# Performance work log

Measured on AMD Instinct MI355X. Metric: run time of the kernel, lower is better.

## Reference

```python
import jax, jax.numpy as jnp
import numpy as np

N_TOKENS = 8192
NQ = 6
NL = 2


def ry_mat(theta):
    # theta: scalar or (B,) -> (2,2) or (B,2,2) complex RY matrix
    c = jnp.cos(theta / 2)
    s = jnp.sin(theta / 2)
    return jnp.stack([jnp.stack([c, -s], -1), jnp.stack([s, c], -1)], -2).astype(jnp.complex64)


def apply_1q(state, gate, q, nq):
    # state: (B, 2**nq); gate: (2,2) shared or (B,2,2) per-batch
    B = state.shape[0]
    st = state.reshape(B, 2 ** q, 2, -1)
    if gate.ndim == 3:
        st = jnp.einsum('bij,bajc->baic', gate, st)
    else:
        st = jnp.einsum('ij,bajc->baic', gate, st)
    return st.reshape(B, -1)


def apply_rz(state, theta, q, nq):
    # diagonal RZ: multiply phases, no matmul needed
    B = state.shape[0]
    st = state.reshape(B, 2 ** q, 2, -1)
    ph = jnp.stack([jnp.exp(-0.5j * theta), jnp.exp(0.5j * theta)]).astype(jnp.complex64)
    return (st * ph[None, None, :, None]).reshape(B, -1)


def apply_cnot(state, c, t, nq):
    B = state.shape[0]
    st = state.reshape((B,) + (2,) * nq)
    s0 = jnp.take(st, 0, axis=1 + c)
    s1 = jnp.take(st, 1, axis=1 + c)
    ta = 1 + t - (1 if t > c else 0)  # target axis after removing control axis
    s1 = jnp.flip(s1, axis=ta)
    st = jnp.stack([s0, s1], axis=1 + c)
    return st.reshape(B, -1)


def prepare_states(x, params, nl, nq):
    # x: (B, nq) angles; params: (nl, nq, 2). Returns (B, 2**nq) complex statevectors.
    B = x.shape[0]
    state = jnp.zeros((B, 2 ** nq), jnp.complex64).at[:, 0].set(1.0)
    for q in range(nq):  # RY angle embedding
        state = apply_1q(state, ry_mat(x[:, q]), q, nq)
    for l in range(nl):  # PQC layers: RY, RZ rotations + CNOT ring
        for q in range(nq):
            state = apply_1q(state, ry_mat(params[l, q, 0]), q, nq)
            state = apply_rz(state, params[l, q, 1], q, nq)
        for q in range(nq):
            state = apply_cnot(state, q, (q + 1) % nq, nq)
    return state


def setup_inputs() -> dict:
    key = jax.random.key(0)
    k1, k2, k3, k4 = jax.random.split(key, 4)
    return {
        'x_tokens': jax.random.normal(k1, (N_TOKENS, NQ), dtype=jnp.float32),
        'params_q': 0.1 * jax.random.normal(k2, (NL, NQ, 2), dtype=jnp.float32),
        'params_k': 0.1 * jax.random.normal(k3, (NL, NQ, 2), dtype=jnp.float32),
        'params_v': 0.1 * jax.random.normal(k4, (NL, NQ, 2), dtype=jnp.float32),
    }


def reference(x_tokens, params_q, params_k, params_v):
    nq = x_tokens.shape[1]
    nl = params_q.shape[0]
    sq = prepare_states(x_tokens, params_q, nl, nq)  # (N, 2**nq)
    sk = prepare_states(x_tokens, params_k, nl, nq)
    ov = jnp.einsum('id,jd->ij', sq, jnp.conj(sk))  # pairwise overlaps (N, N)
    logits = jnp.real(ov * jnp.conj(ov))            # swap-test fidelity |<q|k>|^2
    attn = jax.nn.softmax(logits, axis=-1)
    sv = prepare_states(x_tokens, params_v, nl, nq)
    probs = jnp.real(sv * jnp.conj(sv))             # (N, 2**nq)
    idx = jnp.arange(2 ** nq)
    bits = (idx[None, :] >> (nq - 1 - jnp.arange(nq))[:, None]) & 1  # (nq, 2**nq)
    signs = (1.0 - 2.0 * bits).astype(probs.dtype)
    V = probs @ signs.T                              # <Z_q> per qubit -> (N, nq)
    return attn @ V
```

## Files before the change

kernel.cpp:

```cpp
#include <hip/hip_runtime.h>
#include <hip/hip_bf16.h>

#define NT 8192
#define NQB 6
#define NL 2
#define JSPLIT 16
#define JSLICE (NT / JSPLIT)
#define CHUNK 64
#define NCHUNK (JSLICE / CHUNK)
#define IPW 32
#define WPB 4
#define IPB (IPW * WPB)
#define NBI (NT / IPB)

typedef __bf16 bf16x8 __attribute__((ext_vector_type(8)));
typedef float f32x4 __attribute__((ext_vector_type(4)));

static __device__ __forceinline__ unsigned int pack_bf2(float a, float b) {
  unsigned short lo = __builtin_bit_cast(unsigned short, __float2bfloat16(a));
  unsigned short hi = __builtin_bit_cast(unsigned short, __float2bfloat16(b));
  return (unsigned int)lo | ((unsigned int)hi << 16);
}

static __device__ __forceinline__ int cnot_src(int p, int q) {
  const int mc = 1 << (5 - q);
  const int mt = 1 << (5 - ((q + 1) % NQB));
  return (p & mc) ? (p ^ mt) : p;
}

__global__ __launch_bounds__(256) void prep_kernel(
    const float* __restrict__ x, const float* __restrict__ pq,
    const float* __restrict__ pk, const float* __restrict__ pv,
    unsigned int* __restrict__ Are, unsigned int* __restrict__ Bk,
    float4* __restrict__ V4)
{
  const int wid  = blockIdx.x * 4 + (threadIdx.x >> 6);
  const int lane = threadIdx.x & 63;
  const int set  = wid >> 13;
  const int tok  = wid & (NT - 1);
  const float* pp = (set == 0) ? pq : ((set == 1) ? pk : pv);

  int m = lane;
#pragma unroll
  for (int q = 5; q >= 0; --q) m = cnot_src(m, q);
  int inv = lane;
#pragma unroll
  for (int q = 0; q < 6; ++q) inv = cnot_src(inv, q);

  float R = 1.f, phi = 0.f;
#pragma unroll
  for (int q = 0; q < 6; ++q) {
    float s, c;
    __sincosf(0.5f * (x[tok * NQB + q] + pp[q * 2 + 0]), &s, &c);
    const float bh = 0.5f * pp[q * 2 + 1];
    if ((m >> (5 - q)) & 1) { R *= s; phi += bh; }
    else                    { R *= c; phi -= bh; }
  }
  float sp, cp;
  __sincosf(phi, &sp, &cp);
  float re = R * cp, im = R * sp;

#pragma unroll
  for (int q = 0; q < 6; ++q) {
    const int mask = 1 << (5 - q);
    float s, c;
    __sincosf(0.5f * pp[2 * NQB + q * 2 + 0], &s, &c);
    const float pre = __shfl_xor(re, mask, 64);
    const float pim = __shfl_xor(im, mask, 64);
    const float se = (lane & mask) ? s : -s;
    re = fmaf(se, pre, c * re);
    im = fmaf(se, pim, c * im);
  }
  float phi2 = 0.f;
#pragma unroll
  for (int q = 0; q < 6; ++q) {
    const float bh = 0.5f * pp[2 * NQB + q * 2 + 1];
    phi2 += (lane & (1 << (5 - q))) ? bh : -bh;
  }
  float s2, c2;
  __sincosf(phi2, &s2, &c2);
  const float fre = re * c2 - im * s2;
  const float fim = re * s2 + im * c2;

  if (set == 0) {
    Are[tok * 64 + inv] = pack_bf2(fre, fim);
  } else if (set == 1) {
    Bk[tok * 64 + inv] = pack_bf2(fre, fim);
  } else {
    const float prob = fre * fre + fim * fim;
    float vq[NQB];
#pragma unroll
    for (int q = 0; q < NQB; ++q) {
      float v = (inv & (1 << (5 - q))) ? -prob : prob;
#pragma unroll
      for (int off = 1; off < 64; off <<= 1) v += __shfl_xor(v, off, 64);
      vq[q] = v;
    }
    if (lane == 0) {
      V4[tok * 2 + 0] = make_float4(vq[0], vq[1], vq[2], vq[3]);
      V4[tok * 2 + 1] = make_float4(vq[4], vq[5], 0.f, 0.f);
    }
  }
}

__global__ __launch_bounds__(256, 2) void attn_kernel(
    const uint4* __restrict__ Are, const uint4* __restrict__ Bk,
    const float4* __restrict__ V4, float* __restrict__ part)
{
  __shared__ uint4 kbuf[CHUNK * 17];
  __shared__ float4 vbuf[CHUNK * 2];

  const int tid  = threadIdx.x;
  const int lane = tid & 63;
  const int wave = tid >> 6;
  const int col  = lane & 15;
  const int quad = lane >> 4;

  const int ib = blockIdx.x & (NBI - 1);
  const int js = blockIdx.x / NBI;
  const int ibase = ib * IPB + wave * IPW;
  const int jbase0 = js * JSLICE;

  bf16x8 aRe[2][4], aIm[2][4];
#pragma unroll
  for (int rt = 0; rt < 2; ++rt) {
    const int row = ibase + rt * 16 + col;
    const uint4* pr = Are + row * 16 + quad;
#pragma unroll
    for (int s = 0; s < 4; ++s) {
      const uint4 u = pr[s * 4];
      uint4 w;
      w.x = ((u.x << 16) | (u.x >> 16)) ^ 0x80000000u;
      w.y = ((u.y << 16) | (u.y >> 16)) ^ 0x80000000u;
      w.z = ((u.z << 16) | (u.z >> 16)) ^ 0x80000000u;
      w.w = ((u.w << 16) | (u.w >> 16)) ^ 0x80000000u;
      aRe[rt][s] = __builtin_bit_cast(bf16x8, u);
      aIm[rt][s] = __builtin_bit_cast(bf16x8, w);
    }
  }

  float den[8];
  float num[8][6];
#pragma unroll
  for (int r = 0; r < 8; ++r) {
    den[r] = 0.f;
#pragma unroll
    for (int q = 0; q < 6; ++q) num[r][q] = 0.f;
  }

#pragma unroll 1
  for (int c = 0; c < NCHUNK; ++c) {
    const int jb = jbase0 + c * CHUNK;
    __syncthreads();
#pragma unroll
    for (int r = 0; r < 4; ++r) {
      const int idx = r * 256 + tid;
      kbuf[(idx >> 4) * 17 + (idx & 15)] = Bk[(jb + (idx >> 4)) * 16 + (idx & 15)];
    }
    if (tid < 2 * CHUNK) vbuf[tid] = V4[jb * 2 + tid];
    __syncthreads();

#pragma unroll
    for (int ct = 0; ct < 4; ++ct) {
      const int keyl = ct * 16 + col;
      bf16x8 bfr[4];
#pragma unroll
      for (int s = 0; s < 4; ++s)
        bfr[s] = __builtin_bit_cast(bf16x8, kbuf[keyl * 17 + s * 4 + quad]);
      const float4 v01 = vbuf[keyl * 2 + 0];
      const float4 v23 = vbuf[keyl * 2 + 1];
      const float vv[6] = {v01.x, v01.y, v01.z, v01.w, v23.x, v23.y};
#pragma unroll
      for (int rt = 0; rt < 2; ++rt) {
        f32x4 aR = {0.f, 0.f, 0.f, 0.f};
        f32x4 aI = {0.f, 0.f, 0.f, 0.f};
#pragma unroll
        for (int s = 0; s < 4; ++s) {
          aR = __builtin_amdgcn_mfma_f32_16x16x32_bf16(aRe[rt][s], bfr[s], aR, 0, 0, 0);
          aI = __builtin_amdgcn_mfma_f32_16x16x32_bf16(aIm[rt][s], bfr[s], aI, 0, 0, 0);
        }
#pragma unroll
        for (int r = 0; r < 4; ++r) {
          const float f = aR[r] * aR[r] + aI[r] * aI[r];
          const float w = __expf(f);
          const int rr = rt * 4 + r;
          den[rr] += w;
#pragma unroll
          for (int q = 0; q < 6; ++q) num[rr][q] = fmaf(w, vv[q], num[rr][q]);
        }
      }
    }
  }

#pragma unroll
  for (int rr = 0; rr < 8; ++rr) {
#pragma unroll
    for (int off = 1; off < 16; off <<= 1) {
      den[rr] += __shfl_xor(den[rr], off, 64);
#pragma unroll
      for (int q = 0; q < 6; ++q) num[rr][q] += __shfl_xor(num[rr][q], off, 64);
    }
  }

  if (col == 0) {
#pragma unroll
    for (int rt = 0; rt < 2; ++rt) {
#pragma unroll
      for (int r = 0; r < 4; ++r) {
        const int row = ibase + rt * 16 + quad * 4 + r;
        float* p = part + ((size_t)(js * NT + row)) * 8;
        const int rr = rt * 4 + r;
#pragma unroll
        for (int q = 0; q < 6; ++q) p[q] = num[rr][q];
        p[6] = den[rr];
      }
    }
  }
}

__global__ __launch_bounds__(256) void combine_kernel(
    const float* __restrict__ part, float* __restrict__ out)
{
  const int row = blockIdx.x * 256 + threadIdx.x;
  float acc[7] = {0.f, 0.f, 0.f, 0.f, 0.f, 0.f, 0.f};
#pragma unroll
  for (int js = 0; js < JSPLIT; ++js) {
    const float* p = part + ((size_t)(js * NT + row)) * 8;
#pragma unroll
    for (int q = 0; q < 7; ++q) acc[q] += p[q];
  }
  const float inv = 1.0f / acc[6];
#pragma unroll
  for (int q = 0; q < 6; ++q)
    out[row * 6 + q] = acc[q] * inv;
}

extern "C" void kernel_launch(void* const* d_in, const int* in_sizes, int n_in,
                              void* d_out, int out_size, void* d_ws, size_t ws_size,
                              hipStream_t stream) {
  const float* x  = (const float*)d_in[0];
  const float* pq = (const float*)d_in[1];
  const float* pk = (const float*)d_in[2];
  const float* pv = (const float*)d_in[3];
  char* ws = (char*)d_ws;
  unsigned int* Are = (unsigned int*)(ws);
  unsigned int* Bk  = (unsigned int*)(ws + (size_t)(2u << 20));
  float*        V   = (float*)(ws + (size_t)(4u << 20));
  float*        prt = (float*)(ws + (size_t)(4u << 20) + (size_t)(256u << 10));

  prep_kernel<<<(NT * 3) / 4, 256, 0, stream>>>(x, pq, pk, pv, Are, Bk, (float4*)V);
  attn_kernel<<<NBI * JSPLIT, 256, 0, stream>>>((const uint4*)Are, (const uint4*)Bk,
                                                (const float4*)V, prt);
  combine_kernel<<<NT / 256, 256, 0, stream>>>(prt, (float*)d_out);
}
```

Measured before the change: 129.5 us.

## Fuse split-K combine into attention kernel via atomics and last-block reduction

Removes the separate combine kernel: attention blocks atomically add their partial numerators and denominators into a shared accumulator. A per-row-block counter picks the last finishing block, which normalizes and writes the output. The prep kernel now zeroes the accumulator and counters, and its sincos calls are split into separate __sinf/__cosf. This saves one kernel launch and the partial-buffer round trip, at the cost of atomic contention, an extra fence, and summation order that is no longer deterministic.

```diff
diff --git a/kernel.cpp b/kernel.cpp
--- a/kernel.cpp
+++ b/kernel.cpp
@@ -3,7 +3,6 @@
 
 #define NT 8192
 #define NQB 6
-#define NL 2
 #define JSPLIT 16
 #define JSLICE (NT / JSPLIT)
 #define CHUNK 64
@@ -32,8 +31,14 @@
     const float* __restrict__ x, const float* __restrict__ pq,
     const float* __restrict__ pk, const float* __restrict__ pv,
     unsigned int* __restrict__ Are, unsigned int* __restrict__ Bk,
-    float4* __restrict__ V4)
+    float4* __restrict__ V4, float* __restrict__ acc, int* __restrict__ cnt)
 {
+  if (blockIdx.x < 256) {
+    acc[blockIdx.x * 256 + threadIdx.x] = 0.f;
+  } else if (blockIdx.x == 256 && threadIdx.x < NBI) {
+    cnt[threadIdx.x] = 0;
+  }
+
   const int wid  = blockIdx.x * 4 + (threadIdx.x >> 6);
   const int lane = threadIdx.x & 63;
   const int set  = wid >> 13;
@@ -50,21 +55,19 @@
   float R = 1.f, phi = 0.f;
 #pragma unroll
   for (int q = 0; q < 6; ++q) {
-    float s, c;
-    __sincosf(0.5f * (x[tok * NQB + q] + pp[q * 2 + 0]), &s, &c);
+    const float t = 0.5f * (x[tok * NQB + q] + pp[q * 2 + 0]);
+    const float s = __sinf(t), c = __cosf(t);
     const float bh = 0.5f * pp[q * 2 + 1];
     if ((m >> (5 - q)) & 1) { R *= s; phi += bh; }
     else                    { R *= c; phi -= bh; }
   }
-  float sp, cp;
-  __sincosf(phi, &sp, &cp);
-  float re = R * cp, im = R * sp;
+  float re = R * __cosf(phi), im = R * __sinf(phi);
 
 #pragma unroll
   for (int q = 0; q < 6; ++q) {
     const int mask = 1 << (5 - q);
-    float s, c;
-    __sincosf(0.5f * pp[2 * NQB + q * 2 + 0], &s, &c);
+    const float t = 0.5f * pp[2 * NQB + q * 2 + 0];
+    const float s = __sinf(t), c = __cosf(t);
     const float pre = __shfl_xor(re, mask, 64);
     const float pim = __shfl_xor(im, mask, 64);
     const float se = (lane & mask) ? s : -s;
@@ -77,8 +80,7 @@
     const float bh = 0.5f * pp[2 * NQB + q * 2 + 1];
     phi2 += (lane & (1 << (5 - q))) ? bh : -bh;
   }
-  float s2, c2;
-  __sincosf(phi2, &s2, &c2);
+  const float s2 = __sinf(phi2), c2 = __cosf(phi2);
   const float fre = re * c2 - im * s2;
   const float fim = re * s2 + im * c2;
 
@@ -105,10 +107,12 @@
 
 __global__ __launch_bounds__(256, 2) void attn_kernel(
     const uint4* __restrict__ Are, const uint4* __restrict__ Bk,
-    const float4* __restrict__ V4, float* __restrict__ part)
+    const float4* __restrict__ V4, float* __restrict__ acc,
+    int* __restrict__ cnt, float* __restrict__ out)
 {
   __shared__ uint4 kbuf[CHUNK * 17];
   __shared__ float4 vbuf[CHUNK * 2];
+  __shared__ int lastFlag;
 
   const int tid  = threadIdx.x;
   const int lane = tid & 63;
@@ -208,31 +212,34 @@
 #pragma unroll
       for (int r = 0; r < 4; ++r) {
         const int row = ibase + rt * 16 + quad * 4 + r;
-        float* p = part + ((size_t)(js * NT + row)) * 8;
+        float* a = acc + (size_t)row * 8;
         const int rr = rt * 4 + r;
 #pragma unroll
-        for (int q = 0; q < 6; ++q) p[q] = num[rr][q];
-        p[6] = den[rr];
+        for (int q = 0; q < 6; ++q) atomicAdd(a + q, num[rr][q]);
+        atomicAdd(a + 6, den[rr]);
       }
     }
   }
-}
-
-__global__ __launch_bounds__(256) void combine_kernel(
-    const float* __restrict__ part, float* __restrict__ out)
-{
-  const int row = blockIdx.x * 256 + threadIdx.x;
-  float acc[7] = {0.f, 0.f, 0.f, 0.f, 0.f, 0.f, 0.f};
-#pragma unroll
-  for (int js = 0; js < JSPLIT; ++js) {
-    const float* p = part + ((size_t)(js * NT + row)) * 8;
-#pragma unroll
-    for (int q = 0; q < 7; ++q) acc[q] += p[q];
-  }
-  const float inv = 1.0f / acc[6];
-#pragma unroll
-  for (int q = 0; q < 6; ++q)
-    out[row * 6 + q] = acc[q] * inv;
+
+  __threadfence();
+  __syncthreads();
+  if (tid == 0) lastFlag = (atomicAdd(&cnt[ib], 1) == JSPLIT - 1);
+  __syncthreads();
+  if (lastFlag) {
+    __threadfence();
+    const int ib0 = ib * IPB;
+    for (int r = tid; r < IPB; r += 256) {
+      const int row = ib0 + r;
+      float v[7];
+#pragma unroll
+      for (int q = 0; q < 7; ++q)
+        v[q] = __hip_atomic_load(acc + (size_t)row * 8 + q,
+                                 __ATOMIC_RELAXED, __HIP_MEMORY_SCOPE_AGENT);
+      const float inv = 1.0f / v[6];
+#pragma unroll
+      for (int q = 0; q < 6; ++q) out[row * 6 + q] = v[q] * inv;
+    }
+  }
 }
 
 extern "C" void kernel_launch(void* const* d_in, const int* in_sizes, int n_in,
@@ -245,11 +252,12 @@
   char* ws = (char*)d_ws;
   unsigned int* Are = (unsigned int*)(ws);
   unsigned int* Bk  = (unsigned int*)(ws + (size_t)(2u << 20));
-  float*        V   = (float*)(ws + (size_t)(4u << 20));
-  float*        prt = (float*)(ws + (size_t)(4u << 20) + (size_t)(256u << 10));
-
-  prep_kernel<<<(NT * 3) / 4, 256, 0, stream>>>(x, pq, pk, pv, Are, Bk, (float4*)V);
+  float4*       V4  = (float4*)(ws + (size_t)(4u << 20));
+  float*        acc = (float*)(ws + (size_t)(4u << 20) + (size_t)(256u << 10));
+  int*          cnt = (int*)(ws + (size_t)(4u << 20) + (size_t)(512u << 10));
+
+  prep_kernel<<<(NT * 3) / 4, 256, 0, stream>>>(x, pq, pk, pv, Are, Bk, V4, acc, cnt);
   attn_kernel<<<NBI * JSPLIT, 256, 0, stream>>>((const uint4*)Are, (const uint4*)Bk,
-                                                (const float4*)V, prt);
-  combine_kernel<<<NT / 256, 256, 0, stream>>>(prt, (float*)d_out);
-}
+                                                (const float4*)V4, acc, cnt,
+                                                (float*)d_out);
+}
```

New measurement: 216.8 us. 1.67x slower.
